# Optimization experiments

Measured on AMD Instinct MI355X. Metric: run time of the kernel, lower is better.

Reference implementation:

```python
import jax, jax.numpy as jnp
import numpy as np

B, N, C = 128, 320, 768
H = 12
T = 64    # template tokens (8x8)
S = 256   # search tokens (16x16)


def setup_inputs() -> dict:
    key = jax.random.key(0)
    k1, k2, k3, k4 = jax.random.split(key, 4)
    return {
        "x1": jax.random.normal(k1, (B, N, C), dtype=jnp.float32),
        "x2": jax.random.normal(k2, (B, N, C), dtype=jnp.float32),
        "qkv_w": jax.random.normal(k3, (3 * C, C), dtype=jnp.float32) * 0.02,
        "proj_w": jax.random.normal(k4, (C, C), dtype=jnp.float32) * 0.02,
        "proj_b": jnp.zeros((C,), dtype=jnp.float32),
    }


def reference(x1, x2, qkv_w, proj_w, proj_b):
    # concat template tokens from x1 with search tokens from x2
    x = jnp.concatenate([x1[:, :T, :], x2[:, T:, :]], axis=1)  # [B, N, C]
    b, n, c = x.shape
    d = c // H
    scale = d ** -0.5

    qkv = (x @ qkv_w.T).reshape(b, n, 3, H, d).transpose(2, 0, 3, 1, 4)  # [3,B,H,N,D]
    q, k, v = qkv[0], qkv[1], qkv[2]

    # template -> template self-attention
    q_mt, k_mt, v_mt = q[:, :, :T], k[:, :, :T], v[:, :, :T]
    attn_mt = jax.nn.softmax(jnp.einsum('bhtd,bhsd->bhts', q_mt, k_mt) * scale, axis=-1)
    x_mt = jnp.einsum('bhts,bhsd->bhtd', attn_mt, v_mt).transpose(0, 2, 1, 3).reshape(b, T, c)

    # search -> all cross+self attention
    q_s = q[:, :, T:]
    attn_s = jax.nn.softmax(jnp.einsum('bhqd,bhkd->bhqk', q_s, k) * scale, axis=-1)
    x_s = jnp.einsum('bhqk,bhkd->bhqd', attn_s, v).transpose(0, 2, 1, 3).reshape(b, S, c)

    out = jnp.concatenate([x_mt, x_s], axis=1) @ proj_w.T + proj_b
    return out
```

## Files before the change

### kernel.cpp

```cpp
#include <hip/hip_runtime.h>
#include <hip/hip_bf16.h>
#include <stdint.h>

#define B_   128
#define N_   320
#define C_   768
#define H_   12
#define D_   64
#define NT_  (B_*N_)
#define K3_  (3*C_)
#define NKT  12
#define TE   (256*64)

typedef __attribute__((ext_vector_type(8))) __bf16 bf16x8;
typedef __attribute__((ext_vector_type(4))) float  f32x4;

__device__ __forceinline__ unsigned short f2bf(float f) {
  union { float f; unsigned u; } v; v.f = f;
  return (unsigned short)((v.u + 0x7fffu + ((v.u >> 16) & 1u)) >> 16);
}

__device__ __forceinline__ void gload16(const unsigned short* g, unsigned short* l) {
  __builtin_amdgcn_global_load_lds((const __attribute__((address_space(1))) void*)g,
                                   (__attribute__((address_space(3))) void*)l,
                                   16, 0, 0);
}

__global__ void prep_x(const float* __restrict__ x1, const float* __restrict__ x2,
                       unsigned short* __restrict__ xb) {
  const unsigned total4 = (unsigned)NT_ * C_ / 4;
  const unsigned stride = gridDim.x * blockDim.x;
  for (unsigned i = blockIdx.x * blockDim.x + threadIdx.x; i < total4; i += stride) {
    unsigned tok = i / (C_ / 4);
    unsigned n   = tok % N_;
    const float* src = (n < 64u) ? x1 : x2;
    float4 v = *(const float4*)(src + (size_t)i * 4u);
    ushort4 o;
    o.x = f2bf(v.x); o.y = f2bf(v.y); o.z = f2bf(v.z); o.w = f2bf(v.w);
    *(ushort4*)(xb + (size_t)i * 4u) = o;
  }
}

__global__ void prep_w(const float* __restrict__ qkv_w, const float* __restrict__ proj_w,
                       unsigned short* __restrict__ wq, unsigned short* __restrict__ wp) {
  const int QKV4 = (K3_ * C_) / 4;
  const int Q4   = (C_ * C_) / 4;
  const int P4   = (C_ * C_) / 4;
  int i = blockIdx.x * 256 + threadIdx.x;
  if (i < QKV4) {
    float s = (i < Q4) ? 0.125f : 1.0f;
    float4 v = *(const float4*)(qkv_w + (size_t)i * 4);
    ushort4 o;
    o.x = f2bf(v.x * s); o.y = f2bf(v.y * s); o.z = f2bf(v.z * s); o.w = f2bf(v.w * s);
    *(ushort4*)(wq + (size_t)i * 4) = o;
  } else if (i < QKV4 + P4) {
    int j = i - QKV4;
    float4 v = *(const float4*)(proj_w + (size_t)j * 4);
    ushort4 o;
    o.x = f2bf(v.x); o.y = f2bf(v.y); o.z = f2bf(v.z); o.w = f2bf(v.w);
    *(ushort4*)(wp + (size_t)j * 4) = o;
  }
}

#define BARR do { asm volatile("" ::: "memory"); __builtin_amdgcn_s_barrier(); asm volatile("" ::: "memory"); } while(0)
#define VMW(n) asm volatile("s_waitcnt vmcnt(" #n ")" ::: "memory")
#define PRIO1 __builtin_amdgcn_s_setprio(1)
#define PRIO0 __builtin_amdgcn_s_setprio(0)
#define RD(base, off) (*(const bf16x8*)((base) + (off)))

#define LDA_Q(ARR, QQ, PARX) do { \
    ARR[0][0] = RD(bAk0, (PARX)*32768 + (QQ)*8192);        \
    ARR[0][1] = RD(bAk1, (PARX)*32768 + (QQ)*8192);        \
    ARR[1][0] = RD(bAk0, (PARX)*32768 + (QQ)*8192 + 2048); \
    ARR[1][1] = RD(bAk1, (PARX)*32768 + (QQ)*8192 + 2048); } while(0)

#define LDB(PARX) do { \
    _Pragma("unroll") for (int nf = 0; nf < 4; ++nf) { \
      b_[0][nf] = RD(bBk0, (PARX)*32768 + nf*2048); \
      b_[1][nf] = RD(bBk1, (PARX)*32768 + nf*2048); } } while(0)

#define MFN(ARR, QQ) do { \
    _Pragma("unroll") for (int ks = 0; ks < 2; ++ks) \
    _Pragma("unroll") for (int f = 0; f < 2; ++f) \
    _Pragma("unroll") for (int nf = 0; nf < 4; ++nf) \
      acc[(QQ)*2+f][nf] = __builtin_amdgcn_mfma_f32_16x16x32_bf16(ARR[f][ks], b_[ks][nf], acc[(QQ)*2+f][nf], 0, 0, 0); \
  } while(0)

#define MFS(ARR, QQ) do { \
    _Pragma("unroll") for (int ks = 0; ks < 2; ++ks) \
    _Pragma("unroll") for (int f = 0; f < 2; ++f) \
    _Pragma("unroll") for (int nf = 0; nf < 4; ++nf) \
      acc[(QQ)*2+f][nf] = __builtin_amdgcn_mfma_f32_16x16x32_bf16(b_[ks][nf], ARR[f][ks], acc[(QQ)*2+f][nf], 0, 0, 0); \
  } while(0)

#define STGA4(PARX) do { \
    gload16(gA00, dA + ((PARX)^1)*TE);        gload16(gA01, dA + ((PARX)^1)*TE + 512);  \
    gload16(gA10, dA + ((PARX)^1)*TE + 8192); gload16(gA11, dA + ((PARX)^1)*TE + 8704); \
    gA00 += 64; gA01 += 64; gA10 += 64; gA11 += 64; } while(0)
#define STGB4(PARX) do { \
    gload16(gB00, dB + ((PARX)^1)*TE);        gload16(gB01, dB + ((PARX)^1)*TE + 512);  \
    gload16(gB10, dB + ((PARX)^1)*TE + 8192); gload16(gB11, dB + ((PARX)^1)*TE + 8704); \
    gB00 += 64; gB01 += 64; gB10 += 64; gB11 += 64; } while(0)
#define STG8(PARX) do { STGA4(PARX); STGB4(PARX); } while(0)

#define KT1(MF, PARX, STG_) do { \
    LDB(PARX); LDA_Q(aL_, 0, PARX); \
    STG_; \
    LDA_Q(aH_, 1, PARX); \
    PRIO1; MF(aL_, 0); PRIO0; \
    LDA_Q(aL_, 2, PARX); \
    PRIO1; MF(aH_, 1); PRIO0; \
    LDA_Q(aH_, 3, PARX); \
    PRIO1; MF(aL_, 2); PRIO0; \
    PRIO1; MF(aH_, 3); PRIO0; \
    VMW(0); BARR; \
  } while(0)

#define RESETA do { \
    gA00 = Ag_ + (size_t)row0n*768 + offA00; gA01 = Ag_ + (size_t)row0n*768 + offA01; \
    gA10 = Ag_ + (size_t)row0n*768 + offA10; gA11 = Ag_ + (size_t)row0n*768 + offA11; } while(0)
#define RESETB do { \
    gB00 = Wg_ + (size_t)col0n*768 + offA00; gB01 = Wg_ + (size_t)col0n*768 + offA01; \
    gB10 = Wg_ + (size_t)col0n*768 + offA10; gB11 = Wg_ + (size_t)col0n*768 + offA11; } while(0)

#define TILE12(MF) do { \
    _Pragma("unroll 1") for (int tt = 0; tt < 5; ++tt) { \
      KT1(MF, 0, STG8(0)); \
      KT1(MF, 1, STG8(1)); \
    } \
    KT1(MF, 0, STG8(0)); \
    KT1(MF, 1, { RESETA; RESETB; STG8(1); }); \
  } while(0)

#define GEMM_SETUP \
  const int tid = threadIdx.x, lane = tid & 63, w = tid >> 6; \
  const int wr = w >> 2, wc = w & 3; \
  const int lr = lane & 15, kg = lane >> 4; \
  const int rr = lane >> 3; \
  const int sp = (lane & 7) ^ rr; \
  const char* bAk0 = (const char*)As + wr*4096 + lr*128 + ((0*4 + kg) ^ (lr & 7))*16; \
  const char* bAk1 = (const char*)As + wr*4096 + lr*128 + ((1*4 + kg) ^ (lr & 7))*16; \
  const char* bBk0 = (const char*)Bs + wc*8192 + lr*128 + ((0*4 + kg) ^ (lr & 7))*16; \
  const char* bBk1 = (const char*)Bs + wc*8192 + lr*128 + ((1*4 + kg) ^ (lr & 7))*16; \
  const size_t offA00 = (size_t)(w*16 + rr)*768 + sp*8; \
  const size_t offA01 = offA00 + (size_t)8*768; \
  const size_t offA10 = offA00 + (size_t)128*768; \
  const size_t offA11 = offA01 + (size_t)128*768; \
  unsigned short* dA = As + w*1024; \
  unsigned short* dB = Bs + w*1024; \
  const unsigned short *gA00, *gA01, *gA10, *gA11, *gB00, *gB01, *gB10, *gB11;

#define GEMM_PROLOGUE(row0i, col0i) do { \
    gA00 = Ag_ + (size_t)(row0i)*768 + offA00; gA01 = Ag_ + (size_t)(row0i)*768 + offA01; \
    gA10 = Ag_ + (size_t)(row0i)*768 + offA10; gA11 = Ag_ + (size_t)(row0i)*768 + offA11; \
    gB00 = Wg_ + (size_t)(col0i)*768 + offA00; gB01 = Wg_ + (size_t)(col0i)*768 + offA01; \
    gB10 = Wg_ + (size_t)(col0i)*768 + offA10; gB11 = Wg_ + (size_t)(col0i)*768 + offA11; \
    STG8(1); \
    VMW(0); BARR; \
  } while(0)

#define ACC_ZERO do { \
    _Pragma("unroll") for (int mf = 0; mf < 8; ++mf) \
    _Pragma("unroll") for (int nf = 0; nf < 4; ++nf) acc[mf][nf] = vzero; } while(0)

__global__ void __launch_bounds__(512) gemm_qkv(const unsigned short* __restrict__ A,
                                                const unsigned short* __restrict__ W,
                                                unsigned short* __restrict__ qb,
                                                unsigned short* __restrict__ kb,
                                                unsigned short* __restrict__ vb) {
  __shared__ __align__(16) unsigned short As[2 * TE];
  __shared__ __align__(16) unsigned short Bs[2 * TE];
  GEMM_SETUP
  const unsigned short* Ag_ = A;
  const unsigned short* Wg_ = W;
  const int wv = blockIdx.x / 80;
  const int lb = blockIdx.x - wv * 80;

  const f32x4 vzero = {0.f, 0.f, 0.f, 0.f};
  f32x4 acc[8][4];
  ACC_ZERO;
  bf16x8 aL_[2][2], aH_[2][2], b_[2][4];

  {
    const int t0i = lb * 6;
    const int row0i = (t0i / 3) * 256, col0i = (wv * 3 + t0i % 3) * 256;
    GEMM_PROLOGUE(row0i, col0i);
  }

  if (wv != 2) {
    unsigned short* dst = (wv == 0) ? qb : kb;
#pragma unroll 1
    for (int j = 0; j < 6; ++j) {
      const int t = lb * 6 + j, tn = (j < 5) ? t + 1 : t;
      const int row0c = (t / 3) * 256, cb = (t % 3) * 256;
      const int row0n = (tn / 3) * 256, col0n = (wv * 3 + tn % 3) * 256;
      TILE12(MFS);
#pragma unroll
      for (int mf = 0; mf < 8; ++mf) {
        const int tok = row0c + (mf >> 1) * 64 + wr * 32 + (mf & 1) * 16 + lr;
        const unsigned bq = (unsigned)tok / 320u;
        const int tt2 = tok - (int)bq * 320;
#pragma unroll
        for (int nf = 0; nf < 4; ++nf) {
          const int nn = cb + wc * 64 + nf * 16 + kg * 4;
          const int h = nn >> 6, dd = nn & 63;
          ushort4 o;
          o.x = f2bf(acc[mf][nf][0]); o.y = f2bf(acc[mf][nf][1]);
          o.z = f2bf(acc[mf][nf][2]); o.w = f2bf(acc[mf][nf][3]);
          *(ushort4*)&dst[(size_t)((((int)bq * 12 + h) * 320 + tt2) * 64 + dd)] = o;
        }
      }
      ACC_ZERO;
    }
  } else {
#pragma unroll 1
    for (int j = 0; j < 6; ++j) {
      const int t = lb * 6 + j, tn = (j < 5) ? t + 1 : t;
      const int row0c = (t / 3) * 256, cb = (t % 3) * 256;
      const int row0n = (tn / 3) * 256, col0n = (wv * 3 + tn % 3) * 256;
      TILE12(MFN);
#pragma unroll
      for (int mf = 0; mf < 8; ++mf) {
        const int m0 = row0c + (mf >> 1) * 64 + wr * 32 + (mf & 1) * 16 + kg * 4;
        const unsigned bq = (unsigned)m0 / 320u;
        const int t0v = m0 - (int)bq * 320;
#pragma unroll
        for (int nf = 0; nf < 4; ++nf) {
          const int nn = cb + wc * 64 + nf * 16 + lr;
          const int h = nn >> 6, dd = nn & 63;
          ushort4 o;
          o.x = f2bf(acc[mf][nf][0]); o.y = f2bf(acc[mf][nf][1]);
          o.z = f2bf(acc[mf][nf][2]); o.w = f2bf(acc[mf][nf][3]);
          *(ushort4*)&vb[(size_t)(((((int)bq * 12 + h) * 64 + dd) * 320) + t0v)] = o;
        }
      }
      ACC_ZERO;
    }
  }
  asm volatile("s_waitcnt vmcnt(0) lgkmcnt(0)" ::: "memory");
}

__global__ void __launch_bounds__(256) attn(const unsigned short* __restrict__ qb,
                                            const unsigned short* __restrict__ kb,
                                            const unsigned short* __restrict__ vb,
                                            unsigned short* __restrict__ ab) {
  __shared__ __align__(16) unsigned short Ks[64 * 64];
  __shared__ __align__(16) unsigned short Vt[64 * 64];
  __shared__ __align__(16) unsigned short Pl[4 * 16 * 64];
  const int bid = blockIdx.x;
  const int qt = bid % 5, bh = bid / 5;
  const int tid = threadIdx.x, lane = tid & 63, w = tid >> 6;
  const int lr = lane & 15, kg = lane >> 4;

  const int qrow = qt * 64 + w * 16 + lr;
  const unsigned short* qptr = qb + (bh * 320 + qrow) * 64;
  const bf16x8 qa0 = *(const bf16x8*)(qptr + kg * 8);
  const bf16x8 qa1 = *(const bf16x8*)(qptr + 32 + kg * 8);

  union { unsigned short s[8]; bf16x8 v; } one_u;
#pragma unroll
  for (int i = 0; i < 8; ++i) one_u.s[i] = 0x3F80;
  const bf16x8 vone = one_u.v;

  f32x4 o[4] = {};
  f32x4 accl = {0.f, 0.f, 0.f, 0.f};
  const int nchunk = (qt == 0) ? 1 : 5;

  const int c0 = w, c1 = w + 4;
  const int srow0 = c0 * 8 + (lane >> 3);
  const int srow1 = c1 * 8 + (lane >> 3);
  const int slot  = lane & 7;
  const int part0 = slot ^ (srow0 & 7);
  const int part1 = slot ^ (srow1 & 7);
  const unsigned short* kbase = kb + bh * 320 * 64;
  const unsigned short* vbase = vb + bh * 64 * 320;
  unsigned short* lk0 = &Ks[c0 * 512];
  unsigned short* lk1 = &Ks[c1 * 512];
  unsigned short* lv0 = &Vt[c0 * 512];
  unsigned short* lv1 = &Vt[c1 * 512];
  char* PwB = (char*)&Pl[w * 1024];

  for (int kc = 0; kc < nchunk; kc++) {
    gload16(kbase + (kc * 64 + srow0) * 64 + part0 * 8, lk0);
    gload16(kbase + (kc * 64 + srow1) * 64 + part1 * 8, lk1);
    gload16(vbase + srow0 * 320 + kc * 64 + part0 * 8, lv0);
    gload16(vbase + srow1 * 320 + kc * 64 + part1 * 8, lv1);
    __syncthreads();

    f32x4 s[4];
#pragma unroll
    for (int kt = 0; kt < 4; kt++) {
      const int key = kt * 16 + lr;
      const char* kr = (const char*)Ks + key * 128;
      const unsigned sw = (unsigned)((key & 7) << 4);
      bf16x8 k0 = *(const bf16x8*)(kr + ((kg * 16) ^ sw));
      bf16x8 k1 = *(const bf16x8*)(kr + ((64 + kg * 16) ^ sw));
      f32x4 z = {0.f, 0.f, 0.f, 0.f};
      z = __builtin_amdgcn_mfma_f32_16x16x32_bf16(qa0, k0, z, 0, 0, 0);
      z = __builtin_amdgcn_mfma_f32_16x16x32_bf16(qa1, k1, z, 0, 0, 0);
      s[kt] = z;
    }

#pragma unroll
    for (int r = 0; r < 4; r++) {
      const int q = kg * 4 + r;
      char* prow = PwB + q * 128;
      const unsigned sw = (unsigned)((q & 7) << 4);
#pragma unroll
      for (int kt = 0; kt < 4; kt++) {
        const float p = __expf(s[kt][r]);
        const int key = kt * 16 + lr;
        *(unsigned short*)(prow + ((key * 2) ^ sw)) = f2bf(p);
      }
    }

    asm volatile("s_waitcnt lgkmcnt(0)" ::: "memory");

    {
      const char* par = (const char*)PwB + lr * 128;
      const unsigned swp = (unsigned)((lr & 7) << 4);
      bf16x8 p0 = *(const bf16x8*)(par + ((kg * 16) ^ swp));
      bf16x8 p1 = *(const bf16x8*)(par + ((64 + kg * 16) ^ swp));
#pragma unroll
      for (int dt = 0; dt < 4; dt++) {
        const int d = dt * 16 + lr;
        const char* vr = (const char*)Vt + d * 128;
        const unsigned swv = (unsigned)((d & 7) << 4);
        bf16x8 v0 = *(const bf16x8*)(vr + ((kg * 16) ^ swv));
        bf16x8 v1 = *(const bf16x8*)(vr + ((64 + kg * 16) ^ swv));
        o[dt] = __builtin_amdgcn_mfma_f32_16x16x32_bf16(p0, v0, o[dt], 0, 0, 0);
        o[dt] = __builtin_amdgcn_mfma_f32_16x16x32_bf16(p1, v1, o[dt], 0, 0, 0);
      }
      accl = __builtin_amdgcn_mfma_f32_16x16x32_bf16(p0, vone, accl, 0, 0, 0);
      accl = __builtin_amdgcn_mfma_f32_16x16x32_bf16(p1, vone, accl, 0, 0, 0);
    }
    __syncthreads();
  }

  const int b = bh / 12, h = bh - b * 12;
#pragma unroll
  for (int r = 0; r < 4; r++) {
    const float inv = 1.0f / accl[r];
    const int token = b * 320 + qt * 64 + w * 16 + kg * 4 + r;
    unsigned short* orow = ab + (size_t)token * 768 + h * 64;
#pragma unroll
    for (int dt = 0; dt < 4; dt++)
      orow[dt * 16 + lr] = f2bf(o[dt][r] * inv);
  }
}

__global__ void __launch_bounds__(512) gemm_proj(const unsigned short* __restrict__ A,
                                                 const unsigned short* __restrict__ W,
                                                 const float* __restrict__ bias,
                                                 float* __restrict__ out) {
  __shared__ __align__(16) unsigned short As[2 * TE];
  __shared__ __align__(16) unsigned short Bs[2 * TE];
  GEMM_SETUP
  const unsigned short* Ag_ = A;
  const unsigned short* Wg_ = W;
  const int lb = blockIdx.x;

  const f32x4 vzero = {0.f, 0.f, 0.f, 0.f};
  f32x4 acc[8][4];
  ACC_ZERO;
  bf16x8 aL_[2][2], aH_[2][2], b_[2][4];

  {
    const int t0i = lb * 2;
    const int row0i = (t0i / 3) * 256, col0i = (t0i % 3) * 256;
    GEMM_PROLOGUE(row0i, col0i);
  }

#pragma unroll 1
  for (int j = 0; j < 2; ++j) {
    const int t = lb * 2 + j, tn = (j < 1) ? t + 1 : t;
    const int row0c = (t / 3) * 256, col0c = (t % 3) * 256;
    const int row0n = (tn / 3) * 256, col0n = (tn % 3) * 256;
    TILE12(MFN);
#pragma unroll
    for (int nf = 0; nf < 4; ++nf) {
      const int nn = col0c + wc * 64 + nf * 16 + lr;
      const float bv = bias[nn];
#pragma unroll
      for (int mf = 0; mf < 8; ++mf) {
        const int m0 = row0c + (mf >> 1) * 64 + wr * 32 + (mf & 1) * 16 + kg * 4;
        float* po = out + (size_t)m0 * 768 + nn;
#pragma unroll
        for (int r = 0; r < 4; r++)
          po[(size_t)r * 768] = acc[mf][nf][r] + bv;
      }
    }
    ACC_ZERO;
  }
  asm volatile("s_waitcnt vmcnt(0) lgkmcnt(0)" ::: "memory");
}

extern "C" void kernel_launch(void* const* d_in, const int* in_sizes, int n_in,
                              void* d_out, int out_size, void* d_ws, size_t ws_size,
                              hipStream_t stream) {
  (void)in_sizes; (void)n_in; (void)out_size; (void)ws_size;
  const float* x1     = (const float*)d_in[0];
  const float* x2     = (const float*)d_in[1];
  const float* qkv_w  = (const float*)d_in[2];
  const float* proj_w = (const float*)d_in[3];
  const float* proj_b = (const float*)d_in[4];
  float* out = (float*)d_out;

  const size_t TOK = (size_t)NT_ * C_;
  unsigned short* xb = (unsigned short*)d_ws;
  unsigned short* qb = xb + TOK;
  unsigned short* kb = qb + TOK;
  unsigned short* vb = kb + TOK;
  unsigned short* ab = vb + TOK;
  unsigned short* wq = ab + TOK;
  unsigned short* wp = wq + (size_t)K3_ * C_;

  prep_x<<<8192, 256, 0, stream>>>(x1, x2, xb);
  prep_w<<<2304, 256, 0, stream>>>(qkv_w, proj_w, wq, wp);
  gemm_qkv<<<240, 512, 0, stream>>>(xb, wq, qb, kb, vb);
  attn<<<1536 * 5, 256, 0, stream>>>(qb, kb, vb, ab);
  gemm_proj<<<240, 512, 0, stream>>>(ab, wp, proj_b, out);
}
```

Before: 377.7 us.

## Load GEMM B operand directly from global into registers, drop B LDS staging

Both GEMM kernels stop staging the weight (B) tile through shared memory. Each wave now loads its B fragments straight from global memory into double-buffered registers (b0_/b1_) one k-step ahead, and the Bs LDS arrays are removed. This saves LDS traffic and space and could allow higher occupancy, at the cost of more VGPRs and redundant global loads, since the waves sharing a column slice each fetch the same weights. The attention kernel's block index mapping is also changed so that query tiles are the outer dimension.

After: 539.4 us. 42.8% more time.

```diff
diff --git a/kernel.cpp b/kernel.cpp
--- a/kernel.cpp
+++ b/kernel.cpp
@@ -74,62 +74,55 @@
     ARR[1][0] = RD(bAk0, (PARX)*32768 + (QQ)*8192 + 2048); \
     ARR[1][1] = RD(bAk1, (PARX)*32768 + (QQ)*8192 + 2048); } while(0)
 
-#define LDB(PARX) do { \
+#define LDBG(DST) do { \
     _Pragma("unroll") for (int nf = 0; nf < 4; ++nf) { \
-      b_[0][nf] = RD(bBk0, (PARX)*32768 + nf*2048); \
-      b_[1][nf] = RD(bBk1, (PARX)*32768 + nf*2048); } } while(0)
-
-#define MFN(ARR, QQ) do { \
+      DST[0][nf] = *(const bf16x8*)(gBr + nf*12288); \
+      DST[1][nf] = *(const bf16x8*)(gBr + nf*12288 + 32); } \
+    gBr += 64; } while(0)
+
+#define MFN(ARR, QQ, BB) do { \
     _Pragma("unroll") for (int ks = 0; ks < 2; ++ks) \
     _Pragma("unroll") for (int f = 0; f < 2; ++f) \
     _Pragma("unroll") for (int nf = 0; nf < 4; ++nf) \
-      acc[(QQ)*2+f][nf] = __builtin_amdgcn_mfma_f32_16x16x32_bf16(ARR[f][ks], b_[ks][nf], acc[(QQ)*2+f][nf], 0, 0, 0); \
+      acc[(QQ)*2+f][nf] = __builtin_amdgcn_mfma_f32_16x16x32_bf16(ARR[f][ks], BB[ks][nf], acc[(QQ)*2+f][nf], 0, 0, 0); \
   } while(0)
 
-#define MFS(ARR, QQ) do { \
+#define MFS(ARR, QQ, BB) do { \
     _Pragma("unroll") for (int ks = 0; ks < 2; ++ks) \
     _Pragma("unroll") for (int f = 0; f < 2; ++f) \
     _Pragma("unroll") for (int nf = 0; nf < 4; ++nf) \
-      acc[(QQ)*2+f][nf] = __builtin_amdgcn_mfma_f32_16x16x32_bf16(b_[ks][nf], ARR[f][ks], acc[(QQ)*2+f][nf], 0, 0, 0); \
+      acc[(QQ)*2+f][nf] = __builtin_amdgcn_mfma_f32_16x16x32_bf16(BB[ks][nf], ARR[f][ks], acc[(QQ)*2+f][nf], 0, 0, 0); \
   } while(0)
 
 #define STGA4(PARX) do { \
     gload16(gA00, dA + ((PARX)^1)*TE);        gload16(gA01, dA + ((PARX)^1)*TE + 512);  \
     gload16(gA10, dA + ((PARX)^1)*TE + 8192); gload16(gA11, dA + ((PARX)^1)*TE + 8704); \
     gA00 += 64; gA01 += 64; gA10 += 64; gA11 += 64; } while(0)
-#define STGB4(PARX) do { \
-    gload16(gB00, dB + ((PARX)^1)*TE);        gload16(gB01, dB + ((PARX)^1)*TE + 512);  \
-    gload16(gB10, dB + ((PARX)^1)*TE + 8192); gload16(gB11, dB + ((PARX)^1)*TE + 8704); \
-    gB00 += 64; gB01 += 64; gB10 += 64; gB11 += 64; } while(0)
-#define STG8(PARX) do { STGA4(PARX); STGB4(PARX); } while(0)
-
-#define KT1(MF, PARX, STG_) do { \
-    LDB(PARX); LDA_Q(aL_, 0, PARX); \
+
+#define KT1(MF, PARX, BC, STG_) do { \
+    LDA_Q(aL_, 0, PARX); LDA_Q(aH_, 1, PARX); \
     STG_; \
-    LDA_Q(aH_, 1, PARX); \
-    PRIO1; MF(aL_, 0); PRIO0; \
+    PRIO1; MF(aL_, 0, BC); PRIO0; \
     LDA_Q(aL_, 2, PARX); \
-    PRIO1; MF(aH_, 1); PRIO0; \
+    PRIO1; MF(aH_, 1, BC); PRIO0; \
     LDA_Q(aH_, 3, PARX); \
-    PRIO1; MF(aL_, 2); PRIO0; \
-    PRIO1; MF(aH_, 3); PRIO0; \
+    PRIO1; MF(aL_, 2, BC); PRIO0; \
+    PRIO1; MF(aH_, 3, BC); PRIO0; \
     VMW(0); BARR; \
   } while(0)
 
 #define RESETA do { \
     gA00 = Ag_ + (size_t)row0n*768 + offA00; gA01 = Ag_ + (size_t)row0n*768 + offA01; \
     gA10 = Ag_ + (size_t)row0n*768 + offA10; gA11 = Ag_ + (size_t)row0n*768 + offA11; } while(0)
-#define RESETB do { \
-    gB00 = Wg_ + (size_t)col0n*768 + offA00; gB01 = Wg_ + (size_t)col0n*768 + offA01; \
-    gB10 = Wg_ + (size_t)col0n*768 + offA10; gB11 = Wg_ + (size_t)col0n*768 + offA11; } while(0)
+#define RESETBG (gBr = Wg_ + (size_t)(col0n + wc*64 + lr)*768 + kg*8)
 
 #define TILE12(MF) do { \
     _Pragma("unroll 1") for (int tt = 0; tt < 5; ++tt) { \
-      KT1(MF, 0, STG8(0)); \
-      KT1(MF, 1, STG8(1)); \
+      KT1(MF, 0, b0_, { STGA4(0); LDBG(b1_); }); \
+      KT1(MF, 1, b1_, { STGA4(1); LDBG(b0_); }); \
     } \
-    KT1(MF, 0, STG8(0)); \
-    KT1(MF, 1, { RESETA; RESETB; STG8(1); }); \
+    KT1(MF, 0, b0_, { STGA4(0); LDBG(b1_); }); \
+    KT1(MF, 1, b1_, { RESETA; RESETBG; STGA4(1); LDBG(b0_); }); \
   } while(0)
 
 #define GEMM_SETUP \
@@ -140,22 +133,18 @@
   const int sp = (lane & 7) ^ rr; \
   const char* bAk0 = (const char*)As + wr*4096 + lr*128 + ((0*4 + kg) ^ (lr & 7))*16; \
   const char* bAk1 = (const char*)As + wr*4096 + lr*128 + ((1*4 + kg) ^ (lr & 7))*16; \
-  const char* bBk0 = (const char*)Bs + wc*8192 + lr*128 + ((0*4 + kg) ^ (lr & 7))*16; \
-  const char* bBk1 = (const char*)Bs + wc*8192 + lr*128 + ((1*4 + kg) ^ (lr & 7))*16; \
   const size_t offA00 = (size_t)(w*16 + rr)*768 + sp*8; \
   const size_t offA01 = offA00 + (size_t)8*768; \
   const size_t offA10 = offA00 + (size_t)128*768; \
   const size_t offA11 = offA01 + (size_t)128*768; \
   unsigned short* dA = As + w*1024; \
-  unsigned short* dB = Bs + w*1024; \
-  const unsigned short *gA00, *gA01, *gA10, *gA11, *gB00, *gB01, *gB10, *gB11;
+  const unsigned short *gA00, *gA01, *gA10, *gA11, *gBr;
 
 #define GEMM_PROLOGUE(row0i, col0i) do { \
     gA00 = Ag_ + (size_t)(row0i)*768 + offA00; gA01 = Ag_ + (size_t)(row0i)*768 + offA01; \
     gA10 = Ag_ + (size_t)(row0i)*768 + offA10; gA11 = Ag_ + (size_t)(row0i)*768 + offA11; \
-    gB00 = Wg_ + (size_t)(col0i)*768 + offA00; gB01 = Wg_ + (size_t)(col0i)*768 + offA01; \
-    gB10 = Wg_ + (size_t)(col0i)*768 + offA10; gB11 = Wg_ + (size_t)(col0i)*768 + offA11; \
-    STG8(1); \
+    gBr  = Wg_ + (size_t)((col0i) + wc*64 + lr)*768 + kg*8; \
+    STGA4(1); LDBG(b0_); \
     VMW(0); BARR; \
   } while(0)
 
@@ -169,7 +158,6 @@
                                                 unsigned short* __restrict__ kb,
                                                 unsigned short* __restrict__ vb) {
   __shared__ __align__(16) unsigned short As[2 * TE];
-  __shared__ __align__(16) unsigned short Bs[2 * TE];
   GEMM_SETUP
   const unsigned short* Ag_ = A;
   const unsigned short* Wg_ = W;
@@ -179,7 +167,7 @@
   const f32x4 vzero = {0.f, 0.f, 0.f, 0.f};
   f32x4 acc[8][4];
   ACC_ZERO;
-  bf16x8 aL_[2][2], aH_[2][2], b_[2][4];
+  bf16x8 aL_[2][2], aH_[2][2], b0_[2][4], b1_[2][4];
 
   {
     const int t0i = lb * 6;
@@ -248,7 +236,7 @@
   __shared__ __align__(16) unsigned short Vt[64 * 64];
   __shared__ __align__(16) unsigned short Pl[4 * 16 * 64];
   const int bid = blockIdx.x;
-  const int qt = bid % 5, bh = bid / 5;
+  const int qt = bid / 1536, bh = bid - qt * 1536;
   const int tid = threadIdx.x, lane = tid & 63, w = tid >> 6;
   const int lr = lane & 15, kg = lane >> 4;
 
@@ -354,7 +342,6 @@
                                                  const float* __restrict__ bias,
                                                  float* __restrict__ out) {
   __shared__ __align__(16) unsigned short As[2 * TE];
-  __shared__ __align__(16) unsigned short Bs[2 * TE];
   GEMM_SETUP
   const unsigned short* Ag_ = A;
   const unsigned short* Wg_ = W;
@@ -363,7 +350,7 @@
   const f32x4 vzero = {0.f, 0.f, 0.f, 0.f};
   f32x4 acc[8][4];
   ACC_ZERO;
-  bf16x8 aL_[2][2], aH_[2][2], b_[2][4];
+  bf16x8 aL_[2][2], aH_[2][2], b0_[2][4], b1_[2][4];
 
   {
     const int t0i = lb * 2;
```

## Double-buffer K/V tiles in attention and reorder block index mapping

Applied to the files above, without the earlier changes.

The attention kernel now keeps two LDS buffers for the K and V tiles. It prefetches the next key chunk with global_load_lds while computing on the current one, which overlaps memory latency with the MFMA work. The block-to-(qt,bh) mapping also changes from qt-fastest to bh-fastest, so blocks of the same query tile run together and the single-chunk qt==0 blocks are grouped. LDS use grows, which may lower occupancy, and the loop relies on a VMW wait macro presumably defined earlier in the file.

After: 385.2 us. About the same (+2.0%).

```diff
diff --git a/kernel.cpp b/kernel.cpp
--- a/kernel.cpp
+++ b/kernel.cpp
@@ -244,11 +244,11 @@
                                             const unsigned short* __restrict__ kb,
                                             const unsigned short* __restrict__ vb,
                                             unsigned short* __restrict__ ab) {
-  __shared__ __align__(16) unsigned short Ks[64 * 64];
-  __shared__ __align__(16) unsigned short Vt[64 * 64];
+  __shared__ __align__(16) unsigned short Ks[2 * 64 * 64];
+  __shared__ __align__(16) unsigned short Vt[2 * 64 * 64];
   __shared__ __align__(16) unsigned short Pl[4 * 16 * 64];
   const int bid = blockIdx.x;
-  const int qt = bid % 5, bh = bid / 5;
+  const int qt = bid / 1536, bh = bid - qt * 1536;
   const int tid = threadIdx.x, lane = tid & 63, w = tid >> 6;
   const int lr = lane & 15, kg = lane >> 4;
 
@@ -274,24 +274,34 @@
   const int part1 = slot ^ (srow1 & 7);
   const unsigned short* kbase = kb + bh * 320 * 64;
   const unsigned short* vbase = vb + bh * 64 * 320;
-  unsigned short* lk0 = &Ks[c0 * 512];
-  unsigned short* lk1 = &Ks[c1 * 512];
-  unsigned short* lv0 = &Vt[c0 * 512];
-  unsigned short* lv1 = &Vt[c1 * 512];
   char* PwB = (char*)&Pl[w * 1024];
 
+  gload16(kbase + (srow0) * 64 + part0 * 8, Ks + c0 * 512);
+  gload16(kbase + (srow1) * 64 + part1 * 8, Ks + c1 * 512);
+  gload16(vbase + srow0 * 320 + part0 * 8, Vt + c0 * 512);
+  gload16(vbase + srow1 * 320 + part1 * 8, Vt + c1 * 512);
+  VMW(0);
+  __syncthreads();
+
+#pragma unroll 1
   for (int kc = 0; kc < nchunk; kc++) {
-    gload16(kbase + (kc * 64 + srow0) * 64 + part0 * 8, lk0);
-    gload16(kbase + (kc * 64 + srow1) * 64 + part1 * 8, lk1);
-    gload16(vbase + srow0 * 320 + kc * 64 + part0 * 8, lv0);
-    gload16(vbase + srow1 * 320 + kc * 64 + part1 * 8, lv1);
-    __syncthreads();
+    const int cur = kc & 1;
+    if (kc + 1 < nchunk) {
+      unsigned short* kd = Ks + (cur ^ 1) * 4096;
+      unsigned short* vd = Vt + (cur ^ 1) * 4096;
+      gload16(kbase + ((kc + 1) * 64 + srow0) * 64 + part0 * 8, kd + c0 * 512);
+      gload16(kbase + ((kc + 1) * 64 + srow1) * 64 + part1 * 8, kd + c1 * 512);
+      gload16(vbase + srow0 * 320 + (kc + 1) * 64 + part0 * 8, vd + c0 * 512);
+      gload16(vbase + srow1 * 320 + (kc + 1) * 64 + part1 * 8, vd + c1 * 512);
+    }
+    const char* KsB = (const char*)(Ks + cur * 4096);
+    const char* VtB = (const char*)(Vt + cur * 4096);
 
     f32x4 s[4];
 #pragma unroll
     for (int kt = 0; kt < 4; kt++) {
       const int key = kt * 16 + lr;
-      const char* kr = (const char*)Ks + key * 128;
+      const char* kr = KsB + key * 128;
       const unsigned sw = (unsigned)((key & 7) << 4);
       bf16x8 k0 = *(const bf16x8*)(kr + ((kg * 16) ^ sw));
       bf16x8 k1 = *(const bf16x8*)(kr + ((64 + kg * 16) ^ sw));
@@ -324,7 +334,7 @@
 #pragma unroll
       for (int dt = 0; dt < 4; dt++) {
         const int d = dt * 16 + lr;
-        const char* vr = (const char*)Vt + d * 128;
+        const char* vr = VtB + d * 128;
         const unsigned swv = (unsigned)((d & 7) << 4);
         bf16x8 v0 = *(const bf16x8*)(vr + ((kg * 16) ^ swv));
         bf16x8 v1 = *(const bf16x8*)(vr + ((64 + kg * 16) ^ swv));
@@ -334,6 +344,7 @@
       accl = __builtin_amdgcn_mfma_f32_16x16x32_bf16(p0, vone, accl, 0, 0, 0);
       accl = __builtin_amdgcn_mfma_f32_16x16x32_bf16(p1, vone, accl, 0, 0, 0);
     }
+    VMW(0);
     __syncthreads();
   }
 
```
